# Performance work log

Hardware: AMD Instinct MI355X
Metric: run time of the kernel (lower is better)

Reference implementation:

```python
import jax, jax.numpy as jnp
import numpy as np

NUM_HEADS = 4
HEAD_K = 256
HEAD_V = 512
CHUNK = 64
GATE_NORMALIZER = 16.0
EPS = 1e-5


def _gla_chunk(q, k, v, gk):
    """Chunked gated linear attention.
    q,k,gk: [B,H,S,Dk]; v: [B,H,S,Dv]. gk is log-decay (<=0).
    Recurrence: S_t = diag(exp(gk_t)) S_{t-1} + k_t v_t^T ; o_t = scale * q_t S_t.
    """
    B, H, S, Dk = q.shape
    Dv = v.shape[-1]
    N = S // CHUNK
    scale = Dk ** -0.5

    def to_chunks(x):
        # [B,H,S,D] -> [N,B,H,C,D]
        return x.reshape(B, H, N, CHUNK, x.shape[-1]).transpose(2, 0, 1, 3, 4)

    qc, kc, vc, gkc = map(to_chunks, (q, k, v, gk))
    gc = jnp.cumsum(gkc, axis=-2)  # inclusive cumulative log-decay within chunk

    tri = jnp.tril(jnp.ones((CHUNK, CHUNK), dtype=q.dtype))  # causal incl. diagonal

    def step(Sstate, xs):
        qi, ki, vi, gi = xs  # [B,H,C,Dk]/[B,H,C,Dv]
        q_g = qi * jnp.exp(gi) * scale            # [B,H,C,Dk]
        k_g = ki * jnp.exp(-gi)                   # [B,H,C,Dk]
        A = jnp.einsum('bhid,bhjd->bhij', q_g, k_g) * tri
        o_intra = jnp.einsum('bhij,bhjе->bhiе'.replace('е', 'e'), A, vi)
        o_inter = jnp.einsum('bhcd,bhde->bhce', q_g, Sstate)
        g_last = gi[:, :, -1, :]                  # [B,H,Dk]
        k_dec = ki * jnp.exp(g_last[:, :, None, :] - gi)
        S_new = Sstate * jnp.exp(g_last)[..., None] + jnp.einsum('bhcd,bhce->bhde', k_dec, vi)
        return S_new, o_intra + o_inter

    S0 = jnp.zeros((B, H, Dk, Dv), dtype=q.dtype)
    _, o = jax.lax.scan(step, S0, (qc, kc, vc, gc))
    # [N,B,H,C,Dv] -> [B,H,S,Dv]
    return o.transpose(1, 2, 0, 3, 4).reshape(B, H, S, Dv)


def setup_inputs() -> dict:
    key = jax.random.key(0)
    ks = jax.random.split(key, 10)
    B, S, Hd = 2, 2048, 2048
    key_dim = NUM_HEADS * HEAD_K   # 1024
    value_dim = NUM_HEADS * HEAD_V  # 2048
    lr = 16  # gate_low_rank_dim
    w = lambda k, shp: (jax.random.normal(k, shp, dtype=jnp.float32) * 0.02)
    return {
        'hidden_states': jax.random.normal(ks[0], (B, S, Hd), dtype=jnp.float32),
        'Wq': w(ks[1], (Hd, key_dim)),
        'Wk': w(ks[2], (Hd, key_dim)),
        'Wv': w(ks[3], (Hd, value_dim)),
        'Wgk1': w(ks[4], (Hd, lr)),
        'Wgk2': w(ks[5], (lr, key_dim)),
        'bgk2': jnp.zeros((key_dim,), dtype=jnp.float32),
        'Wg': w(ks[6], (Hd, value_dim)),
        'g_norm_weight': jnp.ones((HEAD_V,), dtype=jnp.float32),
        'Wo': w(ks[7], (value_dim, Hd)),
    }


def reference(hidden_states, Wq, Wk, Wv, Wgk1, Wgk2, bgk2, Wg, g_norm_weight, Wo):
    B, S, Hd = hidden_states.shape
    x = hidden_states
    # projections
    q = (x @ Wq).reshape(B, S, NUM_HEADS, HEAD_K).transpose(0, 2, 1, 3)
    k = (x @ Wk).reshape(B, S, NUM_HEADS, HEAD_K).transpose(0, 2, 1, 3)
    v = (x @ Wv).reshape(B, S, NUM_HEADS, HEAD_V).transpose(0, 2, 1, 3)
    gk = (x @ Wgk1) @ Wgk2 + bgk2
    gk = jax.nn.log_sigmoid(gk) / GATE_NORMALIZER
    gk = gk.reshape(B, S, NUM_HEADS, HEAD_K).transpose(0, 2, 1, 3)

    o = _gla_chunk(q, k, v, gk)  # [B,H,S,Dv]
    o = o.transpose(0, 2, 1, 3)  # [B,S,H,Dv]

    # fused RMSNorm + swish gate
    g = (x @ Wg).reshape(B, S, NUM_HEADS, HEAD_V)
    rms = jnp.sqrt(jnp.mean(o * o, axis=-1, keepdims=True) + EPS)
    o = (o / rms) * g_norm_weight * (g * jax.nn.sigmoid(g))
    o = o.reshape(B, S, NUM_HEADS * HEAD_V)
    return o @ Wo
```

## Files before the change

### kernel.cpp

```cpp
#include <hip/hip_runtime.h>
#include <hip/hip_bf16.h>

#define B_   2
#define S_   2048
#define HD_  2048
#define H_   4
#define DK_  256
#define DV_  512
#define KD_  1024
#define VD_  2048
#define ND_  6144
#define M_   4096
#define NCHUNK_ 32
#define CHUNK_  64

typedef __attribute__((ext_vector_type(8))) short bf16x8;
typedef __attribute__((ext_vector_type(4))) float f32x4;
typedef __attribute__((ext_vector_type(4))) unsigned short us4;
typedef __attribute__((ext_vector_type(8))) unsigned short us8;

__device__ __forceinline__ unsigned short f2bf(float f) {
    __hip_bfloat16 h = __float2bfloat16(f);
    return *reinterpret_cast<unsigned short*>(&h);
}
__device__ __forceinline__ float bf2f(unsigned short u) {
    unsigned int x = ((unsigned int)u) << 16;
    return *reinterpret_cast<float*>(&x);
}

__global__ __launch_bounds__(256) void conv_bf16(const float* __restrict__ in,
                                                 unsigned short* __restrict__ out) {
    const int idx = blockIdx.x * 256 + threadIdx.x;
    float4 a = *(const float4*)&in[(size_t)idx * 4];
    us4 w; w.x = f2bf(a.x); w.y = f2bf(a.y); w.z = f2bf(a.z); w.w = f2bf(a.w);
    *(us4*)&out[(size_t)idx * 4] = w;
}

__global__ __launch_bounds__(256) void tr_w(const float* __restrict__ W,
                                            unsigned short* __restrict__ Wt,
                                            int K, int N) {
    __shared__ float Ws[32][33];
    const int t = threadIdx.x;
    const int n0 = blockIdx.x * 32, k0 = blockIdx.y * 32;
    const int r = t >> 3, c4 = (t & 7) * 4;
    float4 a = *(const float4*)&W[(size_t)(k0 + r) * N + n0 + c4];
    Ws[r][c4 + 0] = a.x; Ws[r][c4 + 1] = a.y; Ws[r][c4 + 2] = a.z; Ws[r][c4 + 3] = a.w;
    __syncthreads();
    const int nr = t >> 3, kc4 = (t & 7) * 4;
    us4 w;
#pragma unroll
    for (int j = 0; j < 4; ++j) w[j] = f2bf(Ws[kc4 + j][nr]);
    *(us4*)&Wt[(size_t)(n0 + nr) * K + k0 + kc4] = w;
}

__global__ __launch_bounds__(256) void tr_v(const unsigned short* __restrict__ qkvg,
                                            unsigned short* __restrict__ vT) {
    __shared__ unsigned short Ws[32][36];
    const int t = threadIdx.x;
    const int c0 = blockIdx.x * 32;
    const int s0 = blockIdx.y * 32;
    {
        const int r = t >> 3, c4 = (t & 7) * 4;
        us4 w = *(const us4*)&qkvg[(size_t)(s0 + r) * ND_ + 2048 + c0 + c4];
        *(us4*)&Ws[r][c4] = w;
    }
    __syncthreads();
    const int er = t >> 3, sc4 = (t & 7) * 4;
    const int c = c0 + er;
    const int h = c >> 9, e = c & 511;
    const int b = s0 >> 11, srow = s0 & 2047;
    us4 w;
#pragma unroll
    for (int j = 0; j < 4; ++j) w[j] = Ws[sc4 + j][er];
    *(us4*)&vT[((size_t)(b * H_ + h) * 512 + e) * 2048 + srow + sc4] = w;
}

__global__ __launch_bounds__(256) void gemm_bt(const unsigned short* __restrict__ A,
                                               const unsigned short* __restrict__ Bt,
                                               float* __restrict__ Cf,
                                               unsigned short* __restrict__ Cb,
                                               int M, int N, int K) {
    __shared__ __align__(16) unsigned short As[128 * 64];
    __shared__ __align__(16) unsigned short Bs[128 * 64];
    const int t = threadIdx.x;
    const int m0 = blockIdx.y * 128, n0 = blockIdx.x * 128;
    const int wave = t >> 6, lane = t & 63;
    const int quad = lane >> 4, l16 = lane & 15;
    const int wm = (wave >> 1) * 64, wn = (wave & 1) * 64;

    f32x4 acc[4][4] = {};

    int aoff[4], boff[4], soff[4];
#pragma unroll
    for (int p = 0; p < 4; ++p) {
        int q = t + p * 256;
        int row = q >> 3, c = (q & 7) * 8;
        soff[p] = row * 64 + (c ^ ((row & 7) * 8));
        aoff[p] = (m0 + row) * K + c;
        boff[p] = (n0 + row) * K + c;
    }

    us8 pa[4], pb[4];
#pragma unroll
    for (int p = 0; p < 4; ++p) {
        pa[p] = *(const us8*)&A[aoff[p]];
        pb[p] = *(const us8*)&Bt[boff[p]];
    }

    for (int k0 = 0; k0 < K; k0 += 64) {
        __syncthreads();
#pragma unroll
        for (int p = 0; p < 4; ++p) {
            *(us8*)&As[soff[p]] = pa[p];
            *(us8*)&Bs[soff[p]] = pb[p];
        }
        __syncthreads();
        if (k0 + 64 < K) {
#pragma unroll
            for (int p = 0; p < 4; ++p) {
                pa[p] = *(const us8*)&A[aoff[p] + k0 + 64];
                pb[p] = *(const us8*)&Bt[boff[p] + k0 + 64];
            }
        }

#pragma unroll
        for (int ks = 0; ks < 2; ++ks) {
            bf16x8 af[4], bfr[4];
#pragma unroll
            for (int i = 0; i < 4; ++i) {
                int r = wm + i * 16 + l16;
                af[i] = *(const bf16x8*)&As[r * 64 + ((ks * 32 + quad * 8) ^ ((r & 7) * 8))];
            }
#pragma unroll
            for (int j = 0; j < 4; ++j) {
                int r = wn + j * 16 + l16;
                bfr[j] = *(const bf16x8*)&Bs[r * 64 + ((ks * 32 + quad * 8) ^ ((r & 7) * 8))];
            }
#pragma unroll
            for (int i = 0; i < 4; ++i)
#pragma unroll
                for (int j = 0; j < 4; ++j)
                    acc[i][j] = __builtin_amdgcn_mfma_f32_16x16x32_bf16(af[i], bfr[j], acc[i][j], 0, 0, 0);
        }
    }

    if (Cb) {
#pragma unroll
        for (int i = 0; i < 4; ++i)
#pragma unroll
            for (int j = 0; j < 4; ++j)
#pragma unroll
                for (int r = 0; r < 4; ++r)
                    Cb[(size_t)(m0 + wm + i * 16 + quad * 4 + r) * N + n0 + wn + j * 16 + l16] = f2bf(acc[i][j][r]);
    } else {
#pragma unroll
        for (int i = 0; i < 4; ++i)
#pragma unroll
            for (int j = 0; j < 4; ++j)
#pragma unroll
                for (int r = 0; r < 4; ++r)
                    Cf[(size_t)(m0 + wm + i * 16 + quad * 4 + r) * N + n0 + wn + j * 16 + l16] = acc[i][j][r];
    }
}

__global__ __launch_bounds__(256) void gemm_n16(const float* __restrict__ X,
                                                const float* __restrict__ W,
                                                float* __restrict__ T) {
    __shared__ float Xs[16][129];
    __shared__ float Wsh[128][17];
    const int t = threadIdx.x;
    const int m0 = blockIdx.x * 16;
    const int mm = t >> 4, jj = t & 15;
    float acc = 0.f;
    for (int k0 = 0; k0 < HD_; k0 += 128) {
        __syncthreads();
#pragma unroll
        for (int p = 0; p < 2; ++p) {
            int q = t + p * 256;
            int r = q >> 5, c4 = (q & 31) * 4;
            float4 a = *(const float4*)&X[(size_t)(m0 + r) * HD_ + k0 + c4];
            Xs[r][c4 + 0] = a.x; Xs[r][c4 + 1] = a.y; Xs[r][c4 + 2] = a.z; Xs[r][c4 + 3] = a.w;
        }
#pragma unroll
        for (int p = 0; p < 8; ++p) {
            int q = t + p * 256;
            int r = q >> 4, c = q & 15;
            Wsh[r][c] = W[(size_t)(k0 + r) * 16 + c];
        }
        __syncthreads();
#pragma unroll 16
        for (int kk = 0; kk < 128; ++kk) acc += Xs[mm][kk] * Wsh[kk][jj];
    }
    T[(size_t)(m0 + mm) * 16 + jj] = acc;
}

__global__ __launch_bounds__(256) void gk_act(const float* __restrict__ T,
                                              const float* __restrict__ W2,
                                              const float* __restrict__ b2,
                                              float* __restrict__ gk) {
    const int idx = blockIdx.x * 256 + threadIdx.x;
    const int n = idx & 1023;
    const int m = idx >> 10;
    float acc = b2[n];
#pragma unroll
    for (int j = 0; j < 16; ++j) acc += T[m * 16 + j] * W2[j * 1024 + n];
    float ls = (acc < 0.f) ? (acc - log1pf(expf(acc))) : (-log1pf(expf(-acc)));
    gk[idx] = ls * 0.0625f;
}

__global__ __launch_bounds__(256) void gate_prep(const unsigned short* __restrict__ qkvg,
                                                 const float* __restrict__ gk,
                                                 unsigned short* __restrict__ qg,
                                                 unsigned short* __restrict__ kg,
                                                 unsigned short* __restrict__ kgT,
                                                 float* __restrict__ glexp) {
    __shared__ unsigned short kgs[64][265];
    const int tid = threadIdx.x;
    const int bhc = blockIdx.x;
    const int chunk = bhc & 31, bh = bhc >> 5;
    const int h = bh & 3, b = bh >> 2;
    const int d = tid;
    const int col = h * 256 + d;
    const size_t row0 = (size_t)b * S_ + chunk * 64;
    const float scale = 0.0625f;
    float gc = 0.f;
    for (int t = 0; t < 64; ++t) {
        size_t r = row0 + t;
        gc += gk[r * (size_t)KD_ + col];
        unsigned short qv = qkvg[r * (size_t)ND_ + col];
        unsigned short kv = qkvg[r * (size_t)ND_ + 1024 + col];
        unsigned short kgv = f2bf(bf2f(kv) * expf(-gc));
        qg[r * (size_t)KD_ + col] = f2bf(bf2f(qv) * expf(gc) * scale);
        kg[r * (size_t)KD_ + col] = kgv;
        kgs[t][d] = kgv;
    }
    glexp[((size_t)bh * 32 + chunk) * 256 + d] = expf(gc);
    __syncthreads();

    const size_t kgTbase = ((size_t)bh * 256) * 2048 + chunk * 64;
#pragma unroll
    for (int p = 0; p < 8; ++p) {
        int q = p * 256 + tid;
        int dd = q >> 3, t8 = (q & 7) * 8;
        us8 w;
#pragma unroll
        for (int i = 0; i < 8; ++i) w[i] = kgs[t8 + i][dd];
        *(us8*)&kgT[kgTbase + (size_t)dd * 2048 + t8] = w;
    }
}

__global__ __launch_bounds__(256) void pass_c1(const unsigned short* __restrict__ qg,
                                               const unsigned short* __restrict__ kg,
                                               unsigned short* __restrict__ Asg) {
    __shared__ __align__(16) unsigned short Aq[64 * 40];
    __shared__ __align__(16) unsigned short Bk[64 * 40];
    const int t = threadIdx.x;
    const int bhc = blockIdx.x;
    const int chunk = bhc & 31, bh = bhc >> 5;
    const int h = bh & 3, b = bh >> 2;
    const int s0 = chunk * 64;
    const int wave = t >> 6, lane = t & 63;
    const int quad = lane >> 4, l16 = lane & 15;
    const int srow = t >> 2, scol = (t & 3) * 8;
    const size_t base = (size_t)b * S_ * KD_ + h * DK_ + (size_t)(s0 + srow) * KD_ + scol;

    f32x4 acc[4] = {};
    us8 aq = *(const us8*)&qg[base];
    us8 bk = *(const us8*)&kg[base];

    for (int k0 = 0; k0 < 256; k0 += 32) {
        __syncthreads();
        *(us8*)&Aq[srow * 40 + scol] = aq;
        *(us8*)&Bk[srow * 40 + scol] = bk;
        __syncthreads();
        if (k0 + 32 < 256) {
            aq = *(const us8*)&qg[base + k0 + 32];
            bk = *(const us8*)&kg[base + k0 + 32];
        }
        bf16x8 bfr = *(const bf16x8*)&Bk[(wave * 16 + l16) * 40 + quad * 8];
#pragma unroll
        for (int i = 0; i < 4; ++i) {
            bf16x8 af = *(const bf16x8*)&Aq[(i * 16 + l16) * 40 + quad * 8];
            acc[i] = __builtin_amdgcn_mfma_f32_16x16x32_bf16(af, bfr, acc[i], 0, 0, 0);
        }
    }

    const int j = wave * 16 + l16;
#pragma unroll
    for (int i = 0; i < 4; ++i)
#pragma unroll
        for (int r = 0; r < 4; ++r) {
            int m = i * 16 + quad * 4 + r;
            float val = (j <= m) ? acc[i][r] : 0.f;
            Asg[(size_t)bhc * 4096 + m * 64 + j] = f2bf(val);
        }
}

__global__ __launch_bounds__(256) void pass_ab(const unsigned short* __restrict__ kgT,
                                               const unsigned short* __restrict__ vT,
                                               const float* __restrict__ gle,
                                               unsigned short* __restrict__ St) {
    __shared__ __align__(16) unsigned short As[64 * 72];
    __shared__ __align__(16) unsigned short Bs[64 * 72];
    const int t = threadIdx.x;
    const int d0 = blockIdx.x * 64;
    const int e0 = blockIdx.y * 64;
    const int bh = blockIdx.z;
    const int wave = t >> 6, lane = t & 63;
    const int quad = lane >> 4, l16 = lane & 15;
    const int wm = (wave >> 1) * 32, wn = (wave & 1) * 32;
    const int srow = t >> 3, sc8 = (t & 7) * 8;

    const size_t vb0 = ((size_t)bh * 512 + e0 + srow) * 2048 + sc8;
    const size_t vb1 = ((size_t)bh * 512 + e0 + 32 + srow) * 2048 + sc8;
    const size_t kb0 = ((size_t)bh * 256 + d0 + srow) * 2048 + sc8;
    const size_t kb1 = ((size_t)bh * 256 + d0 + 32 + srow) * 2048 + sc8;

    f32x4 S[2][2] = {};

    for (int n = 0; n < NCHUNK_; ++n) {
        __syncthreads();
        *(us8*)&As[srow * 72 + sc8]        = *(const us8*)&vT[vb0 + n * 64];
        *(us8*)&As[(srow + 32) * 72 + sc8] = *(const us8*)&vT[vb1 + n * 64];
        *(us8*)&Bs[srow * 72 + sc8]        = *(const us8*)&kgT[kb0 + n * 64];
        *(us8*)&Bs[(srow + 32) * 72 + sc8] = *(const us8*)&kgT[kb1 + n * 64];
        __syncthreads();

        f32x4 acc[2][2] = {};
#pragma unroll
        for (int ks = 0; ks < 2; ++ks) {
            bf16x8 af[2], bfr[2];
#pragma unroll
            for (int i = 0; i < 2; ++i)
                af[i] = *(const bf16x8*)&As[(wm + i * 16 + l16) * 72 + ks * 32 + quad * 8];
#pragma unroll
            for (int j = 0; j < 2; ++j)
                bfr[j] = *(const bf16x8*)&Bs[(wn + j * 16 + l16) * 72 + ks * 32 + quad * 8];
#pragma unroll
            for (int i = 0; i < 2; ++i)
#pragma unroll
                for (int j = 0; j < 2; ++j)
                    acc[i][j] = __builtin_amdgcn_mfma_f32_16x16x32_bf16(af[i], bfr[j], acc[i][j], 0, 0, 0);
        }

        const float E0 = gle[((size_t)bh * 32 + n) * 256 + d0 + wn + l16];
        const float E1 = gle[((size_t)bh * 32 + n) * 256 + d0 + wn + 16 + l16];
        const size_t obase = ((size_t)(bh * 32 + n)) * 512;
#pragma unroll
        for (int i = 0; i < 2; ++i)
#pragma unroll
            for (int j = 0; j < 2; ++j) {
                const float E = j ? E1 : E0;
#pragma unroll
                for (int r = 0; r < 4; ++r) {
                    size_t e = e0 + wm + i * 16 + quad * 4 + r;
                    size_t d = d0 + wn + j * 16 + l16;
                    St[(obase + e) * 256 + d] = f2bf(S[i][j][r]);
                    S[i][j][r] = (S[i][j][r] + acc[i][j][r]) * E;
                }
            }
    }
}

__global__ __launch_bounds__(256) void pass_c2(const unsigned short* __restrict__ qg,
                                               const unsigned short* __restrict__ vT,
                                               const unsigned short* __restrict__ Asg,
                                               const unsigned short* __restrict__ St,
                                               unsigned short* __restrict__ o) {
    __shared__ __align__(16) unsigned short At[64 * 40];
    __shared__ __align__(16) unsigned short Bt[256 * 40];
    const int t = threadIdx.x;
    const int bhc = blockIdx.z;
    const int chunk = bhc & 31, bh = bhc >> 5;
    const int h = bh & 3, b = bh >> 2;
    const int s0 = chunk * 64;
    const int eh = blockIdx.x * 256;
    const int wave = t >> 6, lane = t & 63;
    const int quad = lane >> 4, l16 = lane & 15;
    const int we = wave * 64;

    f32x4 acc[4][4] = {};

    for (int kk0 = 0; kk0 < 10; ++kk0) {
        __syncthreads();
        if (kk0 < 2) {
            {
                int row = t >> 2, c8 = (t & 3) * 8;
                us8 w = *(const us8*)&Asg[(size_t)bhc * 4096 + row * 64 + kk0 * 32 + c8];
                *(us8*)&At[row * 40 + c8] = w;
            }
            const int t0 = kk0 * 32;
#pragma unroll
            for (int p = 0; p < 4; ++p) {
                int q = t + p * 256;
                int row = q >> 2, c8 = (q & 3) * 8;
                us8 w = *(const us8*)&vT[((size_t)bh * 512 + eh + row) * 2048 + s0 + t0 + c8];
                *(us8*)&Bt[row * 40 + c8] = w;
            }
        } else {
            const int d0 = (kk0 - 2) * 32;
            {
                int row = t >> 2, c8 = (t & 3) * 8;
                us8 w = *(const us8*)&qg[((size_t)b * S_ + s0 + row) * KD_ + h * DK_ + d0 + c8];
                *(us8*)&At[row * 40 + c8] = w;
            }
#pragma unroll
            for (int p = 0; p < 4; ++p) {
                int q = t + p * 256;
                int row = q >> 2, c8 = (q & 3) * 8;
                us8 w = *(const us8*)&St[(((size_t)bhc) * 512 + eh + row) * 256 + d0 + c8];
                *(us8*)&Bt[row * 40 + c8] = w;
            }
        }
        __syncthreads();

        bf16x8 af[4], bfr[4];
#pragma unroll
        for (int i = 0; i < 4; ++i)
            af[i] = *(const bf16x8*)&At[(i * 16 + l16) * 40 + quad * 8];
#pragma unroll
        for (int j = 0; j < 4; ++j)
            bfr[j] = *(const bf16x8*)&Bt[(we + j * 16 + l16) * 40 + quad * 8];
#pragma unroll
        for (int i = 0; i < 4; ++i)
#pragma unroll
            for (int j = 0; j < 4; ++j)
                acc[i][j] = __builtin_amdgcn_mfma_f32_16x16x32_bf16(af[i], bfr[j], acc[i][j], 0, 0, 0);
    }

#pragma unroll
    for (int i = 0; i < 4; ++i)
#pragma unroll
        for (int j = 0; j < 4; ++j)
#pragma unroll
            for (int r = 0; r < 4; ++r) {
                int m = i * 16 + quad * 4 + r;
                int e = eh + we + j * 16 + l16;
                o[((size_t)b * S_ + s0 + m) * VD_ + h * DV_ + e] = f2bf(acc[i][j][r]);
            }
}

__global__ __launch_bounds__(256) void postnorm(const unsigned short* __restrict__ o,
                                                const unsigned short* __restrict__ qkvg,
                                                const float* __restrict__ gnw,
                                                unsigned short* __restrict__ obf) {
    const int row = blockIdx.x;
    const int wave = threadIdx.x >> 6;
    const int lane = threadIdx.x & 63;
    const size_t base = (size_t)row * VD_ + wave * 512;
    const size_t gbase = (size_t)row * ND_ + 4096 + wave * 512;
    float x[8];
    float ss = 0.f;
#pragma unroll
    for (int j = 0; j < 8; ++j) {
        x[j] = bf2f(o[base + lane + j * 64]);
        ss += x[j] * x[j];
    }
#pragma unroll
    for (int off = 32; off; off >>= 1) ss += __shfl_xor(ss, off);
    const float inv = 1.0f / sqrtf(ss * (1.0f / 512.0f) + 1e-5f);
#pragma unroll
    for (int j = 0; j < 8; ++j) {
        int e = lane + j * 64;
        float gv = bf2f(qkvg[gbase + e]);
        float sig = 1.0f / (1.0f + expf(-gv));
        obf[base + e] = f2bf(x[j] * inv * gnw[e] * (gv * sig));
    }
}

extern "C" void kernel_launch(void* const* d_in, const int* in_sizes, int n_in,
                              void* d_out, int out_size, void* d_ws, size_t ws_size,
                              hipStream_t stream) {
    const float* x    = (const float*)d_in[0];
    const float* Wq   = (const float*)d_in[1];
    const float* Wk   = (const float*)d_in[2];
    const float* Wv   = (const float*)d_in[3];
    const float* Wgk1 = (const float*)d_in[4];
    const float* Wgk2 = (const float*)d_in[5];
    const float* bgk2 = (const float*)d_in[6];
    const float* Wg   = (const float*)d_in[7];
    const float* gnw  = (const float*)d_in[8];
    const float* Wo   = (const float*)d_in[9];
    float* out = (float*)d_out;

    float* ws = (float*)d_ws;
    const size_t MF = 1048576;
    typedef unsigned short us;
    us* WotT   = (us*)(ws);
    us* qkvg   = (us*)(ws + 2 * MF);
    us* qg     = (us*)(ws + 15 * MF);
    us* kg     = (us*)(ws + 17 * MF);
    us* kgT    = (us*)(ws + 19 * MF);
    us* vT     = (us*)(ws + 21 * MF);
    float* T   = ws + 25 * MF;
    float* gle = T + 65536;
    us* Asg    = (us*)(ws + 25 * MF + 131072);
    us* DtSt   = (us*)(ws + 25 * MF + 786432);
    us* xb     = (us*)(ws + 41 * MF + 786432);
    float* gkb = ws + 41 * MF + 786432;
    us* WcatT  = (us*)(ws + 45 * MF + 786432);
    us* o      = (us*)(ws + 45 * MF + 786432);
    us* obf    = (us*)(ws + 49 * MF + 786432);

    dim3 blk(256);
    conv_bf16<<<8192, blk, 0, stream>>>(x, xb);
    tr_w<<<dim3(32, 64), blk, 0, stream>>>(Wq, WcatT,                   HD_, KD_);
    tr_w<<<dim3(32, 64), blk, 0, stream>>>(Wk, WcatT + 1024 * 2048,     HD_, KD_);
    tr_w<<<dim3(64, 64), blk, 0, stream>>>(Wv, WcatT + 2048 * 2048,     HD_, VD_);
    tr_w<<<dim3(64, 64), blk, 0, stream>>>(Wo, WotT, VD_, HD_);
    tr_w<<<dim3(64, 64), blk, 0, stream>>>(Wg, WcatT + (size_t)4096 * 2048, HD_, VD_);

    gemm_bt<<<dim3(48, 32), blk, 0, stream>>>(xb, WcatT, nullptr, qkvg, M_, ND_, HD_);
    tr_v<<<dim3(64, 128), blk, 0, stream>>>(qkvg, vT);

    gemm_n16<<<M_ / 16, blk, 0, stream>>>(x, Wgk1, T);
    gk_act<<<(M_ * KD_) / 256, blk, 0, stream>>>(T, Wgk2, bgk2, gkb);
    gate_prep<<<256, blk, 0, stream>>>(qkvg, gkb, qg, kg, kgT, gle);

    pass_c1<<<256, blk, 0, stream>>>(qg, kg, Asg);
    pass_ab<<<dim3(4, 8, 8), blk, 0, stream>>>(kgT, vT, gle, DtSt);
    pass_c2<<<dim3(2, 1, 256), blk, 0, stream>>>(qg, vT, Asg, DtSt, o);
    postnorm<<<M_, blk, 0, stream>>>(o, qkvg, gnw, obf);
    gemm_bt<<<dim3(16, 32), blk, 0, stream>>>(obf, WotT, out, nullptr, M_, HD_, VD_);
}
```

Baseline: 476.6 us.

## Merge weight transposes, fuse x conversion, parallelize gate cumsum and state pass

Combines the five weight transpose launches into one kernel and folds the fp32-to-bf16 conversion of x into the low-rank gate GEMM, removing a separate pass over x. gate_prep now uses 1024 threads with a two-level prefix sum to shorten its serial 64-step loop. pass_ab halves its value tile so twice as many blocks run the sequential chunk-state recurrence. The trade-off is more LDS per gate_prep block and less reuse per block in pass_ab.

```diff
diff --git a/kernel.cpp b/kernel.cpp
--- a/kernel.cpp
+++ b/kernel.cpp
@@ -28,20 +28,23 @@
     return *reinterpret_cast<float*>(&x);
 }
 
-__global__ __launch_bounds__(256) void conv_bf16(const float* __restrict__ in,
-                                                 unsigned short* __restrict__ out) {
-    const int idx = blockIdx.x * 256 + threadIdx.x;
-    float4 a = *(const float4*)&in[(size_t)idx * 4];
-    us4 w; w.x = f2bf(a.x); w.y = f2bf(a.y); w.z = f2bf(a.z); w.w = f2bf(a.w);
-    *(us4*)&out[(size_t)idx * 4] = w;
-}
-
-__global__ __launch_bounds__(256) void tr_w(const float* __restrict__ W,
-                                            unsigned short* __restrict__ Wt,
-                                            int K, int N) {
+__global__ __launch_bounds__(256) void tr_w_all(const float* __restrict__ Wq,
+                                                const float* __restrict__ Wk,
+                                                const float* __restrict__ Wv,
+                                                const float* __restrict__ Wg,
+                                                const float* __restrict__ Wo,
+                                                unsigned short* __restrict__ WcatT,
+                                                unsigned short* __restrict__ WotT) {
     __shared__ float Ws[32][33];
     const int t = threadIdx.x;
-    const int n0 = blockIdx.x * 32, k0 = blockIdx.y * 32;
+    const int bx = blockIdx.x;
+    const float* W; unsigned short* Wt; int N, nt;
+    if (bx < 32)       { W = Wq; Wt = WcatT;                        N = 1024; nt = bx; }
+    else if (bx < 64)  { W = Wk; Wt = WcatT + 1024 * 2048;          N = 1024; nt = bx - 32; }
+    else if (bx < 128) { W = Wv; Wt = WcatT + 2048 * 2048;          N = 2048; nt = bx - 64; }
+    else if (bx < 192) { W = Wg; Wt = WcatT + (size_t)4096 * 2048;  N = 2048; nt = bx - 128; }
+    else               { W = Wo; Wt = WotT;                         N = 2048; nt = bx - 192; }
+    const int n0 = nt * 32, k0 = blockIdx.y * 32;
     const int r = t >> 3, c4 = (t & 7) * 4;
     float4 a = *(const float4*)&W[(size_t)(k0 + r) * N + n0 + c4];
     Ws[r][c4 + 0] = a.x; Ws[r][c4 + 1] = a.y; Ws[r][c4 + 2] = a.z; Ws[r][c4 + 3] = a.w;
@@ -50,7 +53,7 @@
     us4 w;
 #pragma unroll
     for (int j = 0; j < 4; ++j) w[j] = f2bf(Ws[kc4 + j][nr]);
-    *(us4*)&Wt[(size_t)(n0 + nr) * K + k0 + kc4] = w;
+    *(us4*)&Wt[(size_t)(n0 + nr) * 2048 + k0 + kc4] = w;
 }
 
 __global__ __launch_bounds__(256) void tr_v(const unsigned short* __restrict__ qkvg,
@@ -165,7 +168,8 @@
 
 __global__ __launch_bounds__(256) void gemm_n16(const float* __restrict__ X,
                                                 const float* __restrict__ W,
-                                                float* __restrict__ T) {
+                                                float* __restrict__ T,
+                                                unsigned short* __restrict__ xb) {
     __shared__ float Xs[16][129];
     __shared__ float Wsh[128][17];
     const int t = threadIdx.x;
@@ -180,6 +184,8 @@
             int r = q >> 5, c4 = (q & 31) * 4;
             float4 a = *(const float4*)&X[(size_t)(m0 + r) * HD_ + k0 + c4];
             Xs[r][c4 + 0] = a.x; Xs[r][c4 + 1] = a.y; Xs[r][c4 + 2] = a.z; Xs[r][c4 + 3] = a.w;
+            us4 wv; wv.x = f2bf(a.x); wv.y = f2bf(a.y); wv.z = f2bf(a.z); wv.w = f2bf(a.w);
+            *(us4*)&xb[(size_t)(m0 + r) * HD_ + k0 + c4] = wv;
         }
 #pragma unroll
         for (int p = 0; p < 8; ++p) {
@@ -208,39 +214,55 @@
     gk[idx] = ls * 0.0625f;
 }
 
-__global__ __launch_bounds__(256) void gate_prep(const unsigned short* __restrict__ qkvg,
-                                                 const float* __restrict__ gk,
-                                                 unsigned short* __restrict__ qg,
-                                                 unsigned short* __restrict__ kg,
-                                                 unsigned short* __restrict__ kgT,
-                                                 float* __restrict__ glexp) {
+__global__ __launch_bounds__(1024) void gate_prep(const unsigned short* __restrict__ qkvg,
+                                                  const float* __restrict__ gk,
+                                                  unsigned short* __restrict__ qg,
+                                                  unsigned short* __restrict__ kg,
+                                                  unsigned short* __restrict__ kgT,
+                                                  float* __restrict__ glexp) {
     __shared__ unsigned short kgs[64][265];
+    __shared__ float psum[4][256];
     const int tid = threadIdx.x;
+    const int d = tid & 255;
+    const int ts = tid >> 8;
     const int bhc = blockIdx.x;
     const int chunk = bhc & 31, bh = bhc >> 5;
     const int h = bh & 3, b = bh >> 2;
-    const int d = tid;
     const int col = h * 256 + d;
-    const size_t row0 = (size_t)b * S_ + chunk * 64;
+    const size_t row0 = (size_t)b * S_ + chunk * 64 + ts * 16;
+
+    float g16[16];
+    float part = 0.f;
+#pragma unroll
+    for (int i = 0; i < 16; ++i) {
+        g16[i] = gk[(row0 + i) * (size_t)KD_ + col];
+        part += g16[i];
+    }
+    psum[ts][d] = part;
+    __syncthreads();
+    float gc = 0.f;
+#pragma unroll
+    for (int j = 0; j < 3; ++j) if (j < ts) gc += psum[j][d];
+
     const float scale = 0.0625f;
-    float gc = 0.f;
-    for (int t = 0; t < 64; ++t) {
-        size_t r = row0 + t;
-        gc += gk[r * (size_t)KD_ + col];
+#pragma unroll
+    for (int i = 0; i < 16; ++i) {
+        gc += g16[i];
+        size_t r = row0 + i;
         unsigned short qv = qkvg[r * (size_t)ND_ + col];
         unsigned short kv = qkvg[r * (size_t)ND_ + 1024 + col];
         unsigned short kgv = f2bf(bf2f(kv) * expf(-gc));
         qg[r * (size_t)KD_ + col] = f2bf(bf2f(qv) * expf(gc) * scale);
         kg[r * (size_t)KD_ + col] = kgv;
-        kgs[t][d] = kgv;
-    }
-    glexp[((size_t)bh * 32 + chunk) * 256 + d] = expf(gc);
+        kgs[ts * 16 + i][d] = kgv;
+    }
+    if (ts == 3) glexp[((size_t)bh * 32 + chunk) * 256 + d] = expf(gc);
     __syncthreads();
 
     const size_t kgTbase = ((size_t)bh * 256) * 2048 + chunk * 64;
 #pragma unroll
-    for (int p = 0; p < 8; ++p) {
-        int q = p * 256 + tid;
+    for (int p = 0; p < 2; ++p) {
+        int q = p * 1024 + tid;
         int dd = q >> 3, t8 = (q & 7) * 8;
         us8 w;
 #pragma unroll
@@ -300,65 +322,56 @@
                                                const unsigned short* __restrict__ vT,
                                                const float* __restrict__ gle,
                                                unsigned short* __restrict__ St) {
-    __shared__ __align__(16) unsigned short As[64 * 72];
+    __shared__ __align__(16) unsigned short As[32 * 72];
     __shared__ __align__(16) unsigned short Bs[64 * 72];
     const int t = threadIdx.x;
     const int d0 = blockIdx.x * 64;
-    const int e0 = blockIdx.y * 64;
+    const int e0 = blockIdx.y * 32;
     const int bh = blockIdx.z;
     const int wave = t >> 6, lane = t & 63;
     const int quad = lane >> 4, l16 = lane & 15;
-    const int wm = (wave >> 1) * 32, wn = (wave & 1) * 32;
+    const int wm = (wave >> 1) * 16;
+    const int wn = (wave & 1) * 32;
     const int srow = t >> 3, sc8 = (t & 7) * 8;
 
-    const size_t vb0 = ((size_t)bh * 512 + e0 + srow) * 2048 + sc8;
-    const size_t vb1 = ((size_t)bh * 512 + e0 + 32 + srow) * 2048 + sc8;
+    const size_t vb  = ((size_t)bh * 512 + e0 + srow) * 2048 + sc8;
     const size_t kb0 = ((size_t)bh * 256 + d0 + srow) * 2048 + sc8;
     const size_t kb1 = ((size_t)bh * 256 + d0 + 32 + srow) * 2048 + sc8;
 
-    f32x4 S[2][2] = {};
+    f32x4 S[2] = {};
 
     for (int n = 0; n < NCHUNK_; ++n) {
         __syncthreads();
-        *(us8*)&As[srow * 72 + sc8]        = *(const us8*)&vT[vb0 + n * 64];
-        *(us8*)&As[(srow + 32) * 72 + sc8] = *(const us8*)&vT[vb1 + n * 64];
+        *(us8*)&As[srow * 72 + sc8]        = *(const us8*)&vT[vb + n * 64];
         *(us8*)&Bs[srow * 72 + sc8]        = *(const us8*)&kgT[kb0 + n * 64];
         *(us8*)&Bs[(srow + 32) * 72 + sc8] = *(const us8*)&kgT[kb1 + n * 64];
         __syncthreads();
 
-        f32x4 acc[2][2] = {};
+        f32x4 acc[2] = {};
 #pragma unroll
         for (int ks = 0; ks < 2; ++ks) {
-            bf16x8 af[2], bfr[2];
-#pragma unroll
-            for (int i = 0; i < 2; ++i)
-                af[i] = *(const bf16x8*)&As[(wm + i * 16 + l16) * 72 + ks * 32 + quad * 8];
-#pragma unroll
-            for (int j = 0; j < 2; ++j)
-                bfr[j] = *(const bf16x8*)&Bs[(wn + j * 16 + l16) * 72 + ks * 32 + quad * 8];
-#pragma unroll
-            for (int i = 0; i < 2; ++i)
-#pragma unroll
-                for (int j = 0; j < 2; ++j)
-                    acc[i][j] = __builtin_amdgcn_mfma_f32_16x16x32_bf16(af[i], bfr[j], acc[i][j], 0, 0, 0);
+            bf16x8 af = *(const bf16x8*)&As[(wm + l16) * 72 + ks * 32 + quad * 8];
+#pragma unroll
+            for (int j = 0; j < 2; ++j) {
+                bf16x8 bfr = *(const bf16x8*)&Bs[(wn + j * 16 + l16) * 72 + ks * 32 + quad * 8];
+                acc[j] = __builtin_amdgcn_mfma_f32_16x16x32_bf16(af, bfr, acc[j], 0, 0, 0);
+            }
         }
 
         const float E0 = gle[((size_t)bh * 32 + n) * 256 + d0 + wn + l16];
         const float E1 = gle[((size_t)bh * 32 + n) * 256 + d0 + wn + 16 + l16];
         const size_t obase = ((size_t)(bh * 32 + n)) * 512;
 #pragma unroll
-        for (int i = 0; i < 2; ++i)
-#pragma unroll
-            for (int j = 0; j < 2; ++j) {
-                const float E = j ? E1 : E0;
-#pragma unroll
-                for (int r = 0; r < 4; ++r) {
-                    size_t e = e0 + wm + i * 16 + quad * 4 + r;
-                    size_t d = d0 + wn + j * 16 + l16;
-                    St[(obase + e) * 256 + d] = f2bf(S[i][j][r]);
-                    S[i][j][r] = (S[i][j][r] + acc[i][j][r]) * E;
-                }
-            }
+        for (int j = 0; j < 2; ++j) {
+            const float E = j ? E1 : E0;
+#pragma unroll
+            for (int r = 0; r < 4; ++r) {
+                size_t e = e0 + wm + quad * 4 + r;
+                size_t d = d0 + wn + j * 16 + l16;
+                St[(obase + e) * 256 + d] = f2bf(S[j][r]);
+                S[j][r] = (S[j][r] + acc[j][r]) * E;
+            }
+        }
     }
 }
 
@@ -503,22 +516,17 @@
     us* obf    = (us*)(ws + 49 * MF + 786432);
 
     dim3 blk(256);
-    conv_bf16<<<8192, blk, 0, stream>>>(x, xb);
-    tr_w<<<dim3(32, 64), blk, 0, stream>>>(Wq, WcatT,                   HD_, KD_);
-    tr_w<<<dim3(32, 64), blk, 0, stream>>>(Wk, WcatT + 1024 * 2048,     HD_, KD_);
-    tr_w<<<dim3(64, 64), blk, 0, stream>>>(Wv, WcatT + 2048 * 2048,     HD_, VD_);
-    tr_w<<<dim3(64, 64), blk, 0, stream>>>(Wo, WotT, VD_, HD_);
-    tr_w<<<dim3(64, 64), blk, 0, stream>>>(Wg, WcatT + (size_t)4096 * 2048, HD_, VD_);
+    gemm_n16<<<M_ / 16, blk, 0, stream>>>(x, Wgk1, T, xb);
+    tr_w_all<<<dim3(256, 64), blk, 0, stream>>>(Wq, Wk, Wv, Wg, Wo, WcatT, WotT);
 
     gemm_bt<<<dim3(48, 32), blk, 0, stream>>>(xb, WcatT, nullptr, qkvg, M_, ND_, HD_);
     tr_v<<<dim3(64, 128), blk, 0, stream>>>(qkvg, vT);
 
-    gemm_n16<<<M_ / 16, blk, 0, stream>>>(x, Wgk1, T);
     gk_act<<<(M_ * KD_) / 256, blk, 0, stream>>>(T, Wgk2, bgk2, gkb);
-    gate_prep<<<256, blk, 0, stream>>>(qkvg, gkb, qg, kg, kgT, gle);
+    gate_prep<<<256, dim3(1024), 0, stream>>>(qkvg, gkb, qg, kg, kgT, gle);
 
     pass_c1<<<256, blk, 0, stream>>>(qg, kg, Asg);
-    pass_ab<<<dim3(4, 8, 8), blk, 0, stream>>>(kgT, vT, gle, DtSt);
+    pass_ab<<<dim3(4, 16, 8), blk, 0, stream>>>(kgT, vT, gle, DtSt);
     pass_c2<<<dim3(2, 1, 256), blk, 0, stream>>>(qg, vT, Asg, DtSt, o);
     postnorm<<<M_, blk, 0, stream>>>(o, qkvg, gnw, obf);
     gemm_bt<<<dim3(16, 32), blk, 0, stream>>>(obf, WotT, out, nullptr, M_, HD_, VD_);
```

After: 439.0 us. 7.9% less time.
